# Performance work log

Measured on AMD Instinct MI355X. Metric: run time of the kernel, lower is better.

The kernel has to match this reference:

```python
import jax, jax.numpy as jnp
import numpy as np

# Module hyperparams (from init_kwargs)
MAX_DISP = 4
DILA = 1
P = 2 * MAX_DISP // DILA + 1  # patch_size = 9 -> 81 output channels


def setup_inputs() -> dict:
    key = jax.random.key(0)
    k0, k1 = jax.random.split(key)
    B, C, H, W = 4, 256, 96, 160
    return {
        "fmap0": jax.random.normal(k0, (B, C, H, W), dtype=jnp.float32),
        "fmap1": jax.random.normal(k1, (B, C, H, W), dtype=jnp.float32),
    }


def reference(fmap0, fmap1):
    """SpatialCorrelationSampler(kernel_size=1, patch_size=P, stride=1,
    padding=0, dilation=1, dilation_patch=DILA), reshaped to (B, P*P, H, W).

    corr[b, p, y, x] = sum_c fmap0[b,c,y,x] * fmap1[b,c,y+dy_p,x+dx_p]
    with (dy,dx) in {-MAX_DISP..MAX_DISP step DILA}; out-of-bounds -> 0
    (no channel normalization, matching the CUDA sampler).
    """
    B, C, H, W = fmap0.shape
    D = MAX_DISP
    # Zero-pad fmap1 so every displacement is a static-size slice.
    padded = jnp.pad(fmap1, ((0, 0), (0, 0), (D, D), (D, D)))
    oy, ox = jnp.meshgrid(jnp.arange(P) * DILA, jnp.arange(P) * DILA, indexing="ij")
    offs = jnp.stack([oy.ravel(), ox.ravel()], axis=1)  # (P*P, 2)

    def one_disp(off):
        # window of fmap1 shifted by (off - D): (B, C, H, W)
        win = jax.lax.dynamic_slice(padded, (0, 0, off[0], off[1]), (B, C, H, W))
        return jnp.einsum("bchw,bchw->bhw", fmap0, win)

    corr = jax.lax.map(one_disp, offs)  # (P*P, B, H, W), avoids P^2*C blowup
    return jnp.transpose(corr, (1, 0, 2, 3))  # (B, P*P, H, W)
```

## Files before the change

### kernel.cpp

```cpp
#include <hip/hip_runtime.h>


#define Bn 4
#define Cn 256
#define Hn 96
#define Wn 160
#define HWn (Hn * Wn)
#define NP 81
#define TY 16
#define TX 16
#define CCH 8
#define NSTAGE (Cn / CCH)
#define WROWS (TY + 8)
#define SEGS 6
#define LROW 32
#define F1C (WROWS * LROW)
#define BUF (CCH * F1C)
#define NT 576
#define F1STG (CCH * HWn / 4)

#define LDS_BAR() asm volatile("s_waitcnt lgkmcnt(0)\n\ts_barrier" ::: "memory")

__global__ __launch_bounds__(NT, 2) void corr_kernel(const float* __restrict__ f0,
                                                     const float* __restrict__ f1,
                                                     float* __restrict__ out) {
    __shared__ __align__(16) float lds[2 * BUF];

    const int tid  = threadIdx.x;
    const int wave = tid >> 6;
    const int lane = tid & 63;
    const int r    = lane >> 2;
    const int g    = lane & 3;

    const int blk = blockIdx.x;
    const int xcd = blk & 7;
    const int it  = blk >> 3;
    const int b   = xcd >> 1;
    const int ty  = (xcd & 1) * 3 + it / 10;
    const int tx  = it % 10;
    const int y0  = ty * TY;
    const int x0  = tx * TX;

    const int scc  = tid / (WROWS * SEGS);
    const int srm  = tid - scc * (WROWS * SEGS);
    const int srr  = srm / SEGS;
    const int sseg = srm - srr * SEGS;
    const int sgy  = y0 - 4 + srr;
    const int sgx  = x0 - 4 + sseg * 4;
    const bool sval = (sgy >= 0) && (sgy < Hn) && (sgx >= 0) && (sgx < Wn);
    const int swz   = (sseg * 4) ^ ((srr & 1) << 4);
    const int slidx = (scc * F1C + srr * LROW + swz) >> 2;
    const int sgidx = sval ? ((((b * Cn + scc) * Hn + sgy) * Wn + sgx) >> 2) : 0;

    const float4* __restrict__ f1v = (const float4*)f1;
    float4* lv = (float4*)lds;

    const int q  = r + wave;
    const int xr = (q & 1) << 4;
    const int o0 = q * LROW + ((g * 4) ^ xr);
    const int o1 = q * LROW + ((g * 4 + 4) ^ xr);
    const int o2 = q * LROW + ((g * 4 + 8) ^ xr);

    float4 p1a = make_float4(0.f, 0.f, 0.f, 0.f), p1b = p1a;
    if (sval) { p1a = f1v[sgidx]; p1b = f1v[sgidx + HWn]; }

    const float* f0s = f0 + ((b * Cn) * Hn + y0 + r) * Wn + x0 + g * 4;
    float4 p0[CCH];
#pragma unroll
    for (int cc = 0; cc < CCH; ++cc) p0[cc] = *(const float4*)(f0s + cc * HWn);

    float acc[9][4];
#pragma unroll
    for (int i = 0; i < 9; ++i)
#pragma unroll
        for (int j = 0; j < 4; ++j) acc[i][j] = 0.f;

    for (int s = 0; s < NSTAGE; ++s) {
        float4* buf = lv + (s & 1) * (BUF / 4);
        buf[slidx]       = p1a;
        buf[slidx + F1C] = p1b;
        LDS_BAR();

        const int ns = (s + 1 < NSTAGE) ? s + 1 : NSTAGE - 1;
        float4 n1a = make_float4(0.f, 0.f, 0.f, 0.f), n1b = n1a;
        if (sval) { n1a = f1v[sgidx + ns * F1STG]; n1b = f1v[sgidx + ns * F1STG + HWn]; }
        float4 n0[CCH];
#pragma unroll
        for (int cc = 0; cc < CCH; ++cc)
            n0[cc] = *(const float4*)(f0s + (ns * CCH + cc) * HWn);
        __builtin_amdgcn_sched_barrier(0);

        const float* base = &lds[(s & 1) * BUF];
#pragma unroll
        for (int cc = 0; cc < CCH; ++cc) {
            const float* wr = base + cc * F1C;
            float4 w0 = *(const float4*)(wr + o0);
            float4 w1 = *(const float4*)(wr + o1);
            float4 w2 = *(const float4*)(wr + o2);
            float av[4]  = {p0[cc].x, p0[cc].y, p0[cc].z, p0[cc].w};
            float wv[12] = {w0.x, w0.y, w0.z, w0.w, w1.x, w1.y, w1.z, w1.w,
                            w2.x, w2.y, w2.z, w2.w};
#pragma unroll
            for (int dx = 0; dx < 9; ++dx)
#pragma unroll
                for (int rx = 0; rx < 4; ++rx)
                    acc[dx][rx] = fmaf(av[rx], wv[rx + dx], acc[dx][rx]);
        }

        p1a = n1a; p1b = n1b;
#pragma unroll
        for (int cc = 0; cc < CCH; ++cc) p0[cc] = n0[cc];
    }

    const int orow = ((b * NP + wave * 9) * Hn + y0 + r) * Wn + x0 + g * 4;
#pragma unroll
    for (int dx = 0; dx < 9; ++dx)
        *(float4*)(out + orow + dx * HWn) =
            make_float4(acc[dx][0], acc[dx][1], acc[dx][2], acc[dx][3]);
}

extern "C" void kernel_launch(void* const* d_in, const int* in_sizes, int n_in,
                              void* d_out, int out_size, void* d_ws, size_t ws_size,
                              hipStream_t stream) {
    const float* f0 = (const float*)d_in[0];
    const float* f1 = (const float*)d_in[1];
    float* out = (float*)d_out;
    corr_kernel<<<dim3(240), NT, 0, stream>>>(f0, f1, out);
}
```

Measured before the change: 197.6 us.

## Split displacement rows across three blocks with smaller 192-thread workgroups

Each block now handles only three of the nine vertical displacement rows, so the grid grows from 240 to 720 blocks of 192 threads. The staged fmap1 window shrinks from 24 to 18 rows, and each thread loads five float4 chunks per stage instead of two. The intent is to fill more CUs and raise occupancy; before, 240 blocks could not cover all compute units. The cost is that fmap0 tiles are reloaded by three blocks each and the overlapping fmap1 rows are fetched redundantly. The custom LDS barrier and sched_barrier were also swapped for a plain __syncthreads.

Result: slower. 215.7 us (+9.2%).

```diff
diff --git a/kernel.cpp b/kernel.cpp
--- a/kernel.cpp
+++ b/kernel.cpp
@@ -11,17 +11,16 @@
 #define TX 16
 #define CCH 8
 #define NSTAGE (Cn / CCH)
-#define WROWS (TY + 8)
+#define WROWS 18
 #define SEGS 6
 #define LROW 32
 #define F1C (WROWS * LROW)
 #define BUF (CCH * F1C)
-#define NT 576
+#define NT 192
+#define STG_TOT (CCH * WROWS * SEGS)
 #define F1STG (CCH * HWn / 4)
 
-#define LDS_BAR() asm volatile("s_waitcnt lgkmcnt(0)\n\ts_barrier" ::: "memory")
-
-__global__ __launch_bounds__(NT, 2) void corr_kernel(const float* __restrict__ f0,
+__global__ __launch_bounds__(NT, 3) void corr_kernel(const float* __restrict__ f0,
                                                      const float* __restrict__ f1,
                                                      float* __restrict__ out) {
     __shared__ __align__(16) float lds[2 * BUF];
@@ -34,23 +33,35 @@
 
     const int blk = blockIdx.x;
     const int xcd = blk & 7;
-    const int it  = blk >> 3;
+    const int idx = blk >> 3;
+    const int it  = idx / 3;
+    const int dg  = idx % 3;
     const int b   = xcd >> 1;
     const int ty  = (xcd & 1) * 3 + it / 10;
     const int tx  = it % 10;
     const int y0  = ty * TY;
     const int x0  = tx * TX;
+    const int dg3 = dg * 3;
 
-    const int scc  = tid / (WROWS * SEGS);
-    const int srm  = tid - scc * (WROWS * SEGS);
-    const int srr  = srm / SEGS;
-    const int sseg = srm - srr * SEGS;
-    const int sgy  = y0 - 4 + srr;
-    const int sgx  = x0 - 4 + sseg * 4;
-    const bool sval = (sgy >= 0) && (sgy < Hn) && (sgx >= 0) && (sgx < Wn);
-    const int swz   = (sseg * 4) ^ ((srr & 1) << 4);
-    const int slidx = (scc * F1C + srr * LROW + swz) >> 2;
-    const int sgidx = sval ? ((((b * Cn + scc) * Hn + sgy) * Wn + sgx) >> 2) : 0;
+    int  slidx[5], sgidx[5];
+    bool sval[5];
+#pragma unroll
+    for (int k = 0; k < 5; ++k) {
+        const int ii  = k * NT + tid;
+        const bool in = (k < 4) || (tid < STG_TOT - 4 * NT);
+        const int scc = ii / (WROWS * SEGS);
+        const int rem = ii - scc * (WROWS * SEGS);
+        const int l   = rem / SEGS;
+        const int seg = rem - l * SEGS;
+        const int gy  = y0 - 4 + dg3 + l;
+        const int gx  = x0 - 4 + seg * 4;
+        sval[k]  = in && (gy >= 0) && (gy < Hn) && (gx >= 0) && (gx < Wn);
+        const int swz = (seg * 4) ^ ((l & 1) << 4);
+        slidx[k] = (scc * F1C + l * LROW + swz) >> 2;
+        sgidx[k] = sval[k] ? ((((b * Cn + scc) * Hn + gy) * Wn + gx) >> 2) : 0;
+        if (!in) slidx[k] = 0;
+    }
+    const bool in4 = (tid < STG_TOT - 4 * NT);
 
     const float4* __restrict__ f1v = (const float4*)f1;
     float4* lv = (float4*)lds;
@@ -61,9 +72,12 @@
     const int o1 = q * LROW + ((g * 4 + 4) ^ xr);
     const int o2 = q * LROW + ((g * 4 + 8) ^ xr);
 
-    float4 p1a = make_float4(0.f, 0.f, 0.f, 0.f), p1b = p1a;
-    if (sval) { p1a = f1v[sgidx]; p1b = f1v[sgidx + HWn]; }
-
+    float4 p1[5];
+#pragma unroll
+    for (int k = 0; k < 5; ++k) {
+        p1[k] = make_float4(0.f, 0.f, 0.f, 0.f);
+        if (sval[k]) p1[k] = f1v[sgidx[k]];
+    }
     const float* f0s = f0 + ((b * Cn) * Hn + y0 + r) * Wn + x0 + g * 4;
     float4 p0[CCH];
 #pragma unroll
@@ -77,18 +91,22 @@
 
     for (int s = 0; s < NSTAGE; ++s) {
         float4* buf = lv + (s & 1) * (BUF / 4);
-        buf[slidx]       = p1a;
-        buf[slidx + F1C] = p1b;
-        LDS_BAR();
+#pragma unroll
+        for (int k = 0; k < 4; ++k) buf[slidx[k]] = p1[k];
+        if (in4) buf[slidx[4]] = p1[4];
+        __syncthreads();
 
         const int ns = (s + 1 < NSTAGE) ? s + 1 : NSTAGE - 1;
-        float4 n1a = make_float4(0.f, 0.f, 0.f, 0.f), n1b = n1a;
-        if (sval) { n1a = f1v[sgidx + ns * F1STG]; n1b = f1v[sgidx + ns * F1STG + HWn]; }
+#pragma unroll
+        for (int k = 0; k < 5; ++k) {
+            float4 t = make_float4(0.f, 0.f, 0.f, 0.f);
+            if (sval[k]) t = f1v[sgidx[k] + ns * F1STG];
+            p1[k] = t;
+        }
         float4 n0[CCH];
 #pragma unroll
         for (int cc = 0; cc < CCH; ++cc)
             n0[cc] = *(const float4*)(f0s + (ns * CCH + cc) * HWn);
-        __builtin_amdgcn_sched_barrier(0);
 
         const float* base = &lds[(s & 1) * BUF];
 #pragma unroll
@@ -107,12 +125,12 @@
                     acc[dx][rx] = fmaf(av[rx], wv[rx + dx], acc[dx][rx]);
         }
 
-        p1a = n1a; p1b = n1b;
 #pragma unroll
         for (int cc = 0; cc < CCH; ++cc) p0[cc] = n0[cc];
     }
 
-    const int orow = ((b * NP + wave * 9) * Hn + y0 + r) * Wn + x0 + g * 4;
+    const int dyi  = dg3 + wave;
+    const int orow = ((b * NP + dyi * 9) * Hn + y0 + r) * Wn + x0 + g * 4;
 #pragma unroll
     for (int dx = 0; dx < 9; ++dx)
         *(float4*)(out + orow + dx * HWn) =
@@ -125,5 +143,5 @@
     const float* f0 = (const float*)d_in[0];
     const float* f1 = (const float*)d_in[1];
     float* out = (float*)d_out;
-    corr_kernel<<<dim3(240), NT, 0, stream>>>(f0, f1, out);
+    corr_kernel<<<dim3(720), NT, 0, stream>>>(f0, f1, out);
 }
```

## Deepen fmap1 prefetch to two stages and store next LDS buffer after compute

Applied to the files above, without the earlier changes.

The fmap1 global loads now run two channel stages ahead, held in registers. The next stage's LDS buffer is written after the current stage's FMAs, followed by one __syncthreads per iteration, instead of writing and then barrier-waiting at the top of the loop. The explicit sched_barrier is removed so the compiler is free to interleave loads with compute. This aims to hide global-load latency and keep the barrier off the critical path, at the cost of extra registers under a 576-thread, 2-blocks-per-CU launch bound.

New measurement: 183.5 us. 1.08x faster.

```diff
diff --git a/kernel.cpp b/kernel.cpp
--- a/kernel.cpp
+++ b/kernel.cpp
@@ -18,8 +18,6 @@
 #define BUF (CCH * F1C)
 #define NT 576
 #define F1STG (CCH * HWn / 4)
-
-#define LDS_BAR() asm volatile("s_waitcnt lgkmcnt(0)\n\ts_barrier" ::: "memory")
 
 __global__ __launch_bounds__(NT, 2) void corr_kernel(const float* __restrict__ f0,
                                                      const float* __restrict__ f1,
@@ -61,8 +59,14 @@
     const int o1 = q * LROW + ((g * 4 + 4) ^ xr);
     const int o2 = q * LROW + ((g * 4 + 8) ^ xr);
 
-    float4 p1a = make_float4(0.f, 0.f, 0.f, 0.f), p1b = p1a;
-    if (sval) { p1a = f1v[sgidx]; p1b = f1v[sgidx + HWn]; }
+    float4 c1a = make_float4(0.f, 0.f, 0.f, 0.f), c1b = c1a;
+    float4 w1a = c1a, w1b = c1a;
+    if (sval) {
+        c1a = f1v[sgidx];            c1b = f1v[sgidx + HWn];
+        w1a = f1v[sgidx + F1STG];    w1b = f1v[sgidx + F1STG + HWn];
+    }
+    lv[slidx]       = c1a;
+    lv[slidx + F1C] = c1b;
 
     const float* f0s = f0 + ((b * Cn) * Hn + y0 + r) * Wn + x0 + g * 4;
     float4 p0[CCH];
@@ -75,20 +79,18 @@
 #pragma unroll
         for (int j = 0; j < 4; ++j) acc[i][j] = 0.f;
 
+    __syncthreads();
+
     for (int s = 0; s < NSTAGE; ++s) {
-        float4* buf = lv + (s & 1) * (BUF / 4);
-        buf[slidx]       = p1a;
-        buf[slidx + F1C] = p1b;
-        LDS_BAR();
+        const int ns2 = (s + 2 < NSTAGE) ? s + 2 : NSTAGE - 1;
+        float4 l1a = make_float4(0.f, 0.f, 0.f, 0.f), l1b = l1a;
+        if (sval) { l1a = f1v[sgidx + ns2 * F1STG]; l1b = f1v[sgidx + ns2 * F1STG + HWn]; }
 
         const int ns = (s + 1 < NSTAGE) ? s + 1 : NSTAGE - 1;
-        float4 n1a = make_float4(0.f, 0.f, 0.f, 0.f), n1b = n1a;
-        if (sval) { n1a = f1v[sgidx + ns * F1STG]; n1b = f1v[sgidx + ns * F1STG + HWn]; }
         float4 n0[CCH];
 #pragma unroll
         for (int cc = 0; cc < CCH; ++cc)
             n0[cc] = *(const float4*)(f0s + (ns * CCH + cc) * HWn);
-        __builtin_amdgcn_sched_barrier(0);
 
         const float* base = &lds[(s & 1) * BUF];
 #pragma unroll
@@ -107,7 +109,14 @@
                     acc[dx][rx] = fmaf(av[rx], wv[rx + dx], acc[dx][rx]);
         }
 
-        p1a = n1a; p1b = n1b;
+        if (s + 1 < NSTAGE) {
+            float4* nbuf = lv + ((s + 1) & 1) * (BUF / 4);
+            nbuf[slidx]       = w1a;
+            nbuf[slidx + F1C] = w1b;
+        }
+        __syncthreads();
+
+        w1a = l1a; w1b = l1b;
 #pragma unroll
         for (int cc = 0; cc < CCH; ++cc) p0[cc] = n0[cc];
     }
```

## Cut register pressure with rolling LDS window buffer and in-loop f0 prefetch

Applied to the files above, without the earlier changes.

Replaces the full next-stage f0 register prefetch with per-channel reloads issued right after each channel's FMAs, and keeps only a 3-deep ring of LDS window reads instead of loading each channel's window just before use. Launch bounds are raised from 2 to 3 blocks per CU, and the custom waitcnt+barrier asm is swapped for __syncthreads. The aim is to lower VGPR usage so more waves can be resident, at the cost of less latency hiding per wave. Only 240 blocks are launched, so higher per-CU occupancy may buy little.

Result: faster. 175.5 us (-11.1%).

```diff
diff --git a/kernel.cpp b/kernel.cpp
--- a/kernel.cpp
+++ b/kernel.cpp
@@ -19,9 +19,7 @@
 #define NT 576
 #define F1STG (CCH * HWn / 4)
 
-#define LDS_BAR() asm volatile("s_waitcnt lgkmcnt(0)\n\ts_barrier" ::: "memory")
-
-__global__ __launch_bounds__(NT, 2) void corr_kernel(const float* __restrict__ f0,
+__global__ __launch_bounds__(NT, 3) void corr_kernel(const float* __restrict__ f0,
                                                      const float* __restrict__ f1,
                                                      float* __restrict__ out) {
     __shared__ __align__(16) float lds[2 * BUF];
@@ -79,37 +77,45 @@
         float4* buf = lv + (s & 1) * (BUF / 4);
         buf[slidx]       = p1a;
         buf[slidx + F1C] = p1b;
-        LDS_BAR();
+        __syncthreads();
 
         const int ns = (s + 1 < NSTAGE) ? s + 1 : NSTAGE - 1;
-        float4 n1a = make_float4(0.f, 0.f, 0.f, 0.f), n1b = n1a;
-        if (sval) { n1a = f1v[sgidx + ns * F1STG]; n1b = f1v[sgidx + ns * F1STG + HWn]; }
-        float4 n0[CCH];
-#pragma unroll
-        for (int cc = 0; cc < CCH; ++cc)
-            n0[cc] = *(const float4*)(f0s + (ns * CCH + cc) * HWn);
+        float4 t1a = make_float4(0.f, 0.f, 0.f, 0.f), t1b = t1a;
+        if (sval) { t1a = f1v[sgidx + ns * F1STG]; t1b = f1v[sgidx + ns * F1STG + HWn]; }
         __builtin_amdgcn_sched_barrier(0);
 
         const float* base = &lds[(s & 1) * BUF];
+        float4 wq[3][3];
+#pragma unroll
+        for (int k = 0; k < 3; ++k) {
+            const float* wr = base + k * F1C;
+            wq[k][0] = *(const float4*)(wr + o0);
+            wq[k][1] = *(const float4*)(wr + o1);
+            wq[k][2] = *(const float4*)(wr + o2);
+        }
+
 #pragma unroll
         for (int cc = 0; cc < CCH; ++cc) {
-            const float* wr = base + cc * F1C;
-            float4 w0 = *(const float4*)(wr + o0);
-            float4 w1 = *(const float4*)(wr + o1);
-            float4 w2 = *(const float4*)(wr + o2);
+            const int sl = cc % 3;
             float av[4]  = {p0[cc].x, p0[cc].y, p0[cc].z, p0[cc].w};
-            float wv[12] = {w0.x, w0.y, w0.z, w0.w, w1.x, w1.y, w1.z, w1.w,
-                            w2.x, w2.y, w2.z, w2.w};
+            float wv[12] = {wq[sl][0].x, wq[sl][0].y, wq[sl][0].z, wq[sl][0].w,
+                            wq[sl][1].x, wq[sl][1].y, wq[sl][1].z, wq[sl][1].w,
+                            wq[sl][2].x, wq[sl][2].y, wq[sl][2].z, wq[sl][2].w};
 #pragma unroll
             for (int dx = 0; dx < 9; ++dx)
 #pragma unroll
                 for (int rx = 0; rx < 4; ++rx)
                     acc[dx][rx] = fmaf(av[rx], wv[rx + dx], acc[dx][rx]);
+            p0[cc] = *(const float4*)(f0s + (ns * CCH + cc) * HWn);
+            if (cc + 3 < CCH) {
+                const float* wr = base + (cc + 3) * F1C;
+                wq[sl][0] = *(const float4*)(wr + o0);
+                wq[sl][1] = *(const float4*)(wr + o1);
+                wq[sl][2] = *(const float4*)(wr + o2);
+            }
         }
 
-        p1a = n1a; p1b = n1b;
-#pragma unroll
-        for (int cc = 0; cc < CCH; ++cc) p0[cc] = n0[cc];
+        p1a = t1a; p1b = t1b;
     }
 
     const int orow = ((b * NP + wave * 9) * Hn + y0 + r) * Wn + x0 + g * 4;
```
